# Performance work log

Measured on AMD Instinct MI355X. Metric: run time of the kernel, lower is better.

## Reference

```python
import jax, jax.numpy as jnp
import numpy as np

B, S, D, H = 2, 2048, 1024, 16
DK = D // H
NEG = -1e9


def setup_inputs() -> dict:
    key = jax.random.key(0)
    ks = jax.random.split(key, 12)
    inp = {
        "query": jax.random.normal(ks[0], (B, S, D), jnp.float32),
        "key": jax.random.normal(ks[1], (B, S, D), jnp.float32),
        "value": jax.random.normal(ks[2], (B, S, D), jnp.float32),
        "mask": jax.random.randint(ks[3], (B, S), 0, 2, jnp.int32),
    }
    # 4 linears (q, k, v, out), each d_model x d_model with bias.
    scale = 1.0 / np.sqrt(D)
    for i, name in enumerate(["wq", "wk", "wv", "wo"]):
        inp[name] = jax.random.uniform(ks[4 + i], (D, D), jnp.float32, -scale, scale)
        inp["b" + name[1]] = jax.random.uniform(ks[8 + i], (D,), jnp.float32, -scale, scale)
    return inp


def _split_heads(x):  # [B,S,D] -> [B,H,S,DK]
    return x.reshape(B, S, H, DK).transpose(0, 2, 1, 3)


def reference(query, key, value, mask, wq, bq, wk, bk, wv, bv, wo, bo):
    q = _split_heads(query @ wq.T + bq)
    k = _split_heads(key @ wk.T + bk)
    v = _split_heads(value @ wv.T + bv)
    scores = jnp.einsum("bhqd,bhkd->bhqk", q, k) / jnp.sqrt(jnp.float32(DK))
    # mask: [B,S] -> [B,1,1,S]; masked_fill where mask == 0
    m = mask[:, None, None, :]
    scores = jnp.where(m == 0, NEG, scores)
    attn = jax.nn.softmax(scores, axis=-1)  # dropout p=0 (eval) -> identity
    x = jnp.einsum("bhqk,bhkd->bhqd", attn, v)
    x = x.transpose(0, 2, 1, 3).reshape(B, S, D)
    return x @ wo.T + bo
```

## Files before the change

### kernel.cpp

```cpp
#include <hip/hip_runtime.h>


typedef _Float16 f16;
typedef _Float16 f16x8 __attribute__((ext_vector_type(8)));
typedef _Float16 f16x4 __attribute__((ext_vector_type(4)));
typedef float f32x4 __attribute__((ext_vector_type(4)));

#define MFMA_F16(a, b, c) __builtin_amdgcn_mfma_f32_16x16x32_f16((a), (b), (c), 0, 0, 0)
#define MFMA16(a, b, c) __builtin_amdgcn_mfma_f32_16x16x16f16((a), (b), (c), 0, 0, 0)
#define L2E 1.44269504088896340736f

__device__ __forceinline__ void gld16(const void* g, void* l) {
    __builtin_amdgcn_global_load_lds(
        (__attribute__((address_space(1))) void*)(g),
        (__attribute__((address_space(3))) void*)(l), 16, 0, 0);
}

__global__ __launch_bounds__(256) void cvt_kernel(
    const float* __restrict__ q, const float* __restrict__ k,
    const float* __restrict__ v,
    const float* __restrict__ wq, const float* __restrict__ wk,
    const float* __restrict__ wv, const float* __restrict__ wo,
    f16* __restrict__ oq, f16* __restrict__ ok, f16* __restrict__ ov,
    f16* __restrict__ owq, f16* __restrict__ owk, f16* __restrict__ owv,
    f16* __restrict__ owo)
{
    const int z = blockIdx.y;
    const float* src;
    f16* dst;
    int n;
    switch (z) {
        case 0: src = q;  dst = oq;  n = 4194304; break;
        case 1: src = k;  dst = ok;  n = 4194304; break;
        case 2: src = v;  dst = ov;  n = 4194304; break;
        case 3: src = wq; dst = owq; n = 1048576; break;
        case 4: src = wk; dst = owk; n = 1048576; break;
        case 5: src = wv; dst = owv; n = 1048576; break;
        default: src = wo; dst = owo; n = 1048576; break;
    }
    int idx = (blockIdx.x * 256 + threadIdx.x) * 8;
    if (idx >= n) return;
    float4 a = *(const float4*)(src + idx);
    float4 b = *(const float4*)(src + idx + 4);
    f16x8 h = { (f16)a.x, (f16)a.y, (f16)a.z, (f16)a.w,
                (f16)b.x, (f16)b.y, (f16)b.z, (f16)b.w };
    *(f16x8*)(dst + idx) = h;
}

__global__ __launch_bounds__(256) void proj_qkv_kernel(
    const f16* __restrict__ xq, const f16* __restrict__ xk,
    const f16* __restrict__ xv,
    const f16* __restrict__ wqh, const f16* __restrict__ wkh,
    const f16* __restrict__ wvh,
    const float* __restrict__ bq, const float* __restrict__ bk,
    const float* __restrict__ bv,
    f16* __restrict__ qh, f16* __restrict__ kh, f16* __restrict__ vt)
{
    const int z = blockIdx.z;
    const f16* X = (z == 0) ? xq : (z == 1) ? xk : xv;
    const f16* W = (z == 0) ? wqh : (z == 1) ? wkh : wvh;
    const float* bias = (z == 0) ? bq : (z == 1) ? bk : bv;
    const f16* P0 = (z < 2) ? W : X;
    const f16* P1 = (z < 2) ? X : W;

    __shared__ __align__(16) f16 As[128 * 64];
    __shared__ __align__(16) f16 Bs[128 * 64];

    const int t = threadIdx.x;
    const int wave = t >> 6, lane = t & 63, quad = lane >> 4, l15 = lane & 15;
    const int m_base = (wave >> 1) * 64, n_base = (wave & 1) * 64;
    const int blockM = (z < 2) ? blockIdx.x * 128 : blockIdx.y * 128;
    const int blockN = (z < 2) ? blockIdx.y * 128 : blockIdx.x * 128;

    const int srow = lane >> 3;
    const int sblk = (lane & 7) ^ srow;

    f32x4 acc[4][4];
#pragma unroll
    for (int mt = 0; mt < 4; mt++)
#pragma unroll
        for (int nt = 0; nt < 4; nt++)
            acc[mt][nt] = (f32x4){0.f, 0.f, 0.f, 0.f};

    for (int k0 = 0; k0 < 1024; k0 += 64) {
        __syncthreads();
#pragma unroll
        for (int j = 0; j < 4; j++) {
            int r0 = wave * 32 + j * 8;
            gld16(&P0[(size_t)(blockM + r0 + srow) * 1024 + k0 + sblk * 8],
                  &As[r0 * 64]);
            gld16(&P1[(size_t)(blockN + r0 + srow) * 1024 + k0 + sblk * 8],
                  &Bs[r0 * 64]);
        }
        __syncthreads();

#pragma unroll
        for (int c = 0; c < 2; c++) {
            f16x8 af[4], bf[4];
#pragma unroll
            for (int mt = 0; mt < 4; mt++)
                af[mt] = *(const f16x8*)(&As[(m_base + mt * 16 + l15) * 64 +
                                             (((c * 4 + quad) ^ (l15 & 7)) << 3)]);
#pragma unroll
            for (int nt = 0; nt < 4; nt++)
                bf[nt] = *(const f16x8*)(&Bs[(n_base + nt * 16 + l15) * 64 +
                                             (((c * 4 + quad) ^ (l15 & 7)) << 3)]);
#pragma unroll
            for (int mt = 0; mt < 4; mt++)
#pragma unroll
                for (int nt = 0; nt < 4; nt++)
                    acc[mt][nt] = MFMA_F16(af[mt], bf[nt], acc[mt][nt]);
        }
    }

    if (z < 2) {
        f16* o = (z == 0) ? qh : kh;
        const float scale = (z == 0) ? 0.125f * L2E : 1.0f;
#pragma unroll
        for (int mt = 0; mt < 4; mt++) {
            int j0 = blockM + m_base + mt * 16 + quad * 4;
            float4 b4 = *(const float4*)(&bias[j0]);
            int h = j0 >> 6, dk = j0 & 63;
#pragma unroll
            for (int nt = 0; nt < 4; nt++) {
                int s_g = blockN + n_base + nt * 16 + l15;
                int b = s_g >> 11, s = s_g & 2047;
                f16x4 pk = { (f16)((acc[mt][nt][0] + b4.x) * scale),
                             (f16)((acc[mt][nt][1] + b4.y) * scale),
                             (f16)((acc[mt][nt][2] + b4.z) * scale),
                             (f16)((acc[mt][nt][3] + b4.w) * scale) };
                *(f16x4*)(&o[(((size_t)(b * 16 + h) * 2048 + s) << 6) + dk]) = pk;
            }
        }
    } else {
        float bv_[4];
#pragma unroll
        for (int nt = 0; nt < 4; nt++)
            bv_[nt] = bias[blockN + n_base + nt * 16 + l15];
#pragma unroll
        for (int mt = 0; mt < 4; mt++) {
            int row0 = blockM + m_base + mt * 16 + quad * 4;
            int b = row0 >> 11, s0 = row0 & 2047;
#pragma unroll
            for (int nt = 0; nt < 4; nt++) {
                int col_g = blockN + n_base + nt * 16 + l15;
                int h = col_g >> 6, dk = col_g & 63;
                f16x4 pk = { (f16)(acc[mt][nt][0] + bv_[nt]),
                             (f16)(acc[mt][nt][1] + bv_[nt]),
                             (f16)(acc[mt][nt][2] + bv_[nt]),
                             (f16)(acc[mt][nt][3] + bv_[nt]) };
                *(f16x4*)(&vt[((size_t)((b * 16 + h) * 64 + dk) << 11) + s0]) = pk;
            }
        }
    }
}

__global__ __launch_bounds__(256) void flash_kernel(
    const f16* __restrict__ qh, const f16* __restrict__ kh,
    const f16* __restrict__ vt, const int* __restrict__ mask,
    f16* __restrict__ ctx)
{
    __shared__ __align__(16) f16 Ks[64 * 64];
    __shared__ __align__(16) f16 Vts[64 * 64];
    __shared__ float bias_s[64];

    const int t = threadIdx.x;
    const int wave = t >> 6, lane = t & 63, quad = lane >> 4, l15 = lane & 15;
    const int bh = blockIdx.y;
    const int b = bh >> 4, h = bh & 15;
    const int q0 = blockIdx.x * 128;

    const f16* qbase = qh + (size_t)bh * (2048 * 64);
    const f16* kbase = kh + (size_t)bh * (2048 * 64);
    const f16* vbase = vt + (size_t)bh * (64 * 2048);

    f16x8 qf[2][2];
#pragma unroll
    for (int cb = 0; cb < 2; cb++) {
        int qrow = q0 + wave * 32 + cb * 16 + l15;
        qf[cb][0] = *(const f16x8*)(&qbase[qrow * 64 + quad * 8]);
        qf[cb][1] = *(const f16x8*)(&qbase[qrow * 64 + 32 + quad * 8]);
    }

    f32x4 O[2][4];
#pragma unroll
    for (int cb = 0; cb < 2; cb++)
#pragma unroll
        for (int n = 0; n < 4; n++) O[cb][n] = (f32x4){0.f, 0.f, 0.f, 0.f};
    float l_part[2] = {0.f, 0.f};

    const int sr = t >> 3;
    const int sb = t & 7;

    for (int kt = 0; kt < 32; kt++) {
        __syncthreads();
        const int key0 = kt * 64;
#pragma unroll
        for (int p = 0; p < 2; p++) {
            int row = p * 32 + sr;
            int pb = (sb ^ (row & 7)) << 3;
            *(f16x8*)(&Ks[row * 64 + pb]) =
                *(const f16x8*)(&kbase[(key0 + row) * 64 + sb * 8]);
            *(f16x8*)(&Vts[row * 64 + pb]) =
                *(const f16x8*)(&vbase[row * 2048 + key0 + sb * 8]);
        }
        if (t < 64)
            bias_s[t] = (mask[b * 2048 + key0 + t] == 0) ? -1.0e9f : 0.0f;
        __syncthreads();

        f32x4 sc[2][4];
#pragma unroll
        for (int nt = 0; nt < 4; nt++) {
            const f16* krow = &Ks[(nt * 16 + l15) * 64];
            f16x8 kf0 = *(const f16x8*)(&krow[(quad ^ (l15 & 7)) << 3]);
            f16x8 kf1 = *(const f16x8*)(&krow[((quad + 4) ^ (l15 & 7)) << 3]);
            float4 b4 = *(const float4*)(&bias_s[nt * 16 + quad * 4]);
#pragma unroll
            for (int cb = 0; cb < 2; cb++) {
                f32x4 z4 = (f32x4){b4.x, b4.y, b4.z, b4.w};
                z4 = MFMA_F16(kf0, qf[cb][0], z4);
                sc[cb][nt] = MFMA_F16(kf1, qf[cb][1], z4);
            }
        }

        f16x4 pf[2][4];
#pragma unroll
        for (int cb = 0; cb < 2; cb++) {
            float rs = 0.f;
#pragma unroll
            for (int nt = 0; nt < 4; nt++)
#pragma unroll
                for (int i = 0; i < 4; i++) {
                    float p = exp2f(sc[cb][nt][i]);
                    rs += p;
                    pf[cb][nt][i] = (f16)p;
                }
            l_part[cb] += rs;
        }

#pragma unroll
        for (int nto = 0; nto < 4; nto++) {
            const f16* vrow = &Vts[(nto * 16 + l15) * 64];
#pragma unroll
            for (int nt = 0; nt < 4; nt++) {
                f16x4 vf = *(const f16x4*)(&vrow[
                    (((nt * 2 + (quad >> 1)) ^ (l15 & 7)) << 3) + (quad & 1) * 4]);
                O[0][nto] = MFMA16(vf, pf[0][nt], O[0][nto]);
                O[1][nto] = MFMA16(vf, pf[1][nt], O[1][nto]);
            }
        }
    }

#pragma unroll
    for (int cb = 0; cb < 2; cb++) {
        float l = l_part[cb];
        l += __shfl_xor(l, 16);
        l += __shfl_xor(l, 32);
        const float inv_l = 1.0f / l;
        int qrow = q0 + wave * 32 + cb * 16 + l15;
#pragma unroll
        for (int nto = 0; nto < 4; nto++) {
            f16x4 pk = { (f16)(O[cb][nto][0] * inv_l),
                         (f16)(O[cb][nto][1] * inv_l),
                         (f16)(O[cb][nto][2] * inv_l),
                         (f16)(O[cb][nto][3] * inv_l) };
            *(f16x4*)(&ctx[(size_t)(b * 2048 + qrow) * 1024 + h * 64 +
                           nto * 16 + quad * 4]) = pk;
        }
    }
}

__global__ __launch_bounds__(256) void proj_out_kernel(
    const f16* __restrict__ ctx, const f16* __restrict__ woh,
    const float* __restrict__ bo, float* __restrict__ out)
{
    __shared__ __align__(16) f16 As[128 * 64];
    __shared__ __align__(16) f16 Bs[128 * 64];

    const int t = threadIdx.x;
    const int wave = t >> 6, lane = t & 63, quad = lane >> 4, l15 = lane & 15;
    const int m_base = (wave >> 1) * 64, n_base = (wave & 1) * 64;
    const int blockM = blockIdx.y * 128, blockN = blockIdx.x * 128;

    const int srow = lane >> 3;
    const int sblk = (lane & 7) ^ srow;

    f32x4 acc[4][4];
#pragma unroll
    for (int mt = 0; mt < 4; mt++)
#pragma unroll
        for (int nt = 0; nt < 4; nt++)
            acc[mt][nt] = (f32x4){0.f, 0.f, 0.f, 0.f};

    for (int k0 = 0; k0 < 1024; k0 += 64) {
        __syncthreads();
#pragma unroll
        for (int j = 0; j < 4; j++) {
            int r0 = wave * 32 + j * 8;
            gld16(&ctx[(size_t)(blockM + r0 + srow) * 1024 + k0 + sblk * 8],
                  &As[r0 * 64]);
            gld16(&woh[(size_t)(blockN + r0 + srow) * 1024 + k0 + sblk * 8],
                  &Bs[r0 * 64]);
        }
        __syncthreads();

#pragma unroll
        for (int c = 0; c < 2; c++) {
            f16x8 af[4], bf[4];
#pragma unroll
            for (int mt = 0; mt < 4; mt++)
                af[mt] = *(const f16x8*)(&As[(m_base + mt * 16 + l15) * 64 +
                                             (((c * 4 + quad) ^ (l15 & 7)) << 3)]);
#pragma unroll
            for (int nt = 0; nt < 4; nt++)
                bf[nt] = *(const f16x8*)(&Bs[(n_base + nt * 16 + l15) * 64 +
                                             (((c * 4 + quad) ^ (l15 & 7)) << 3)]);
#pragma unroll
            for (int mt = 0; mt < 4; mt++)
#pragma unroll
                for (int nt = 0; nt < 4; nt++)
                    acc[mt][nt] = MFMA_F16(af[mt], bf[nt], acc[mt][nt]);
        }
    }

    float bo_[4];
#pragma unroll
    for (int nt = 0; nt < 4; nt++)
        bo_[nt] = bo[blockN + n_base + nt * 16 + l15];

#pragma unroll
    for (int mt = 0; mt < 4; mt++) {
        int row0 = blockM + m_base + mt * 16 + quad * 4;
#pragma unroll
        for (int nt = 0; nt < 4; nt++) {
            int col_g = blockN + n_base + nt * 16 + l15;
#pragma unroll
            for (int i = 0; i < 4; i++)
                out[(size_t)(row0 + i) * 1024 + col_g] = acc[mt][nt][i] + bo_[nt];
        }
    }
}

extern "C" void kernel_launch(void* const* d_in, const int* in_sizes, int n_in,
                              void* d_out, int out_size, void* d_ws, size_t ws_size,
                              hipStream_t stream) {
    const float* query = (const float*)d_in[0];
    const float* key_  = (const float*)d_in[1];
    const float* value = (const float*)d_in[2];
    const int*   mask  = (const int*)d_in[3];
    const float* wq = (const float*)d_in[4];
    const float* bq = (const float*)d_in[5];
    const float* wk = (const float*)d_in[6];
    const float* bk = (const float*)d_in[7];
    const float* wv = (const float*)d_in[8];
    const float* bv = (const float*)d_in[9];
    const float* wo = (const float*)d_in[10];
    const float* bo = (const float*)d_in[11];
    float* out = (float*)d_out;

    f16* xq  = (f16*)d_ws;
    f16* xk  = xq  + 4194304;
    f16* xv  = xk  + 4194304;
    f16* wqh = xv  + 4194304;
    f16* wkh = wqh + 1048576;
    f16* wvh = wkh + 1048576;
    f16* woh = wvh + 1048576;
    f16* qh  = woh + 1048576;
    f16* kh  = qh  + 4194304;
    f16* vt  = kh  + 4194304;
    f16* ctx = xq;

    cvt_kernel<<<dim3(2048, 7), 256, 0, stream>>>(
        query, key_, value, wq, wk, wv, wo, xq, xk, xv, wqh, wkh, wvh, woh);
    proj_qkv_kernel<<<dim3(8, 32, 3), 256, 0, stream>>>(
        xq, xk, xv, wqh, wkh, wvh, bq, bk, bv, qh, kh, vt);
    flash_kernel<<<dim3(16, 32), 256, 0, stream>>>(qh, kh, vt, mask, ctx);
    proj_out_kernel<<<dim3(8, 32), 256, 0, stream>>>(ctx, woh, bo, out);
}
```

Before: 260.0 us.

## Swap grid axes for L2 locality, use direct-to-LDS loads and precompute mask bias

Transposes the launch grids of the projection and attention kernels so consecutive blocks share the same weight or head data, which is meant to improve L2 reuse. The flash kernel now stages K and V tiles with global_load_lds instead of going through registers. It also builds the whole mask bias row (2048 floats) in LDS once per block rather than once per key tile. This costs extra LDS, which may reduce occupancy.

```diff
diff --git a/kernel.cpp b/kernel.cpp
--- a/kernel.cpp
+++ b/kernel.cpp
@@ -69,8 +69,8 @@
     const int t = threadIdx.x;
     const int wave = t >> 6, lane = t & 63, quad = lane >> 4, l15 = lane & 15;
     const int m_base = (wave >> 1) * 64, n_base = (wave & 1) * 64;
-    const int blockM = (z < 2) ? blockIdx.x * 128 : blockIdx.y * 128;
-    const int blockN = (z < 2) ? blockIdx.y * 128 : blockIdx.x * 128;
+    const int blockM = (z < 2) ? blockIdx.y * 128 : blockIdx.x * 128;
+    const int blockN = (z < 2) ? blockIdx.x * 128 : blockIdx.y * 128;
 
     const int srow = lane >> 3;
     const int sblk = (lane & 7) ^ srow;
@@ -162,17 +162,23 @@
 {
     __shared__ __align__(16) f16 Ks[64 * 64];
     __shared__ __align__(16) f16 Vts[64 * 64];
-    __shared__ float bias_s[64];
+    __shared__ float bias_all[2048];
 
     const int t = threadIdx.x;
     const int wave = t >> 6, lane = t & 63, quad = lane >> 4, l15 = lane & 15;
-    const int bh = blockIdx.y;
+    const int bh = blockIdx.x;
     const int b = bh >> 4, h = bh & 15;
-    const int q0 = blockIdx.x * 128;
+    const int q0 = blockIdx.y * 128;
 
     const f16* qbase = qh + (size_t)bh * (2048 * 64);
     const f16* kbase = kh + (size_t)bh * (2048 * 64);
     const f16* vbase = vt + (size_t)bh * (64 * 2048);
+
+#pragma unroll
+    for (int j = 0; j < 8; j++) {
+        int i = j * 256 + t;
+        bias_all[i] = (mask[b * 2048 + i] == 0) ? -1.0e9f : 0.0f;
+    }
 
     f16x8 qf[2][2];
 #pragma unroll
@@ -189,23 +195,19 @@
         for (int n = 0; n < 4; n++) O[cb][n] = (f32x4){0.f, 0.f, 0.f, 0.f};
     float l_part[2] = {0.f, 0.f};
 
-    const int sr = t >> 3;
-    const int sb = t & 7;
+    const int srow8 = lane >> 3;
+    const int sblk = (lane & 7) ^ srow8;
 
     for (int kt = 0; kt < 32; kt++) {
         __syncthreads();
         const int key0 = kt * 64;
 #pragma unroll
         for (int p = 0; p < 2; p++) {
-            int row = p * 32 + sr;
-            int pb = (sb ^ (row & 7)) << 3;
-            *(f16x8*)(&Ks[row * 64 + pb]) =
-                *(const f16x8*)(&kbase[(key0 + row) * 64 + sb * 8]);
-            *(f16x8*)(&Vts[row * 64 + pb]) =
-                *(const f16x8*)(&vbase[row * 2048 + key0 + sb * 8]);
-        }
-        if (t < 64)
-            bias_s[t] = (mask[b * 2048 + key0 + t] == 0) ? -1.0e9f : 0.0f;
+            int r0 = p * 32 + wave * 8;
+            int row = r0 + srow8;
+            gld16(&kbase[(size_t)(key0 + row) * 64 + sblk * 8], &Ks[r0 * 64]);
+            gld16(&vbase[(size_t)row * 2048 + key0 + sblk * 8], &Vts[r0 * 64]);
+        }
         __syncthreads();
 
         f32x4 sc[2][4];
@@ -214,7 +216,7 @@
             const f16* krow = &Ks[(nt * 16 + l15) * 64];
             f16x8 kf0 = *(const f16x8*)(&krow[(quad ^ (l15 & 7)) << 3]);
             f16x8 kf1 = *(const f16x8*)(&krow[((quad + 4) ^ (l15 & 7)) << 3]);
-            float4 b4 = *(const float4*)(&bias_s[nt * 16 + quad * 4]);
+            float4 b4 = *(const float4*)(&bias_all[key0 + nt * 16 + quad * 4]);
 #pragma unroll
             for (int cb = 0; cb < 2; cb++) {
                 f32x4 z4 = (f32x4){b4.x, b4.y, b4.z, b4.w};
@@ -280,7 +282,8 @@
     const int t = threadIdx.x;
     const int wave = t >> 6, lane = t & 63, quad = lane >> 4, l15 = lane & 15;
     const int m_base = (wave >> 1) * 64, n_base = (wave & 1) * 64;
-    const int blockM = blockIdx.y * 128, blockN = blockIdx.x * 128;
+    const int blockM = blockIdx.x * 128;
+    const int blockN = blockIdx.y * 128;
 
     const int srow = lane >> 3;
     const int sblk = (lane & 7) ^ srow;
@@ -372,8 +375,8 @@
 
     cvt_kernel<<<dim3(2048, 7), 256, 0, stream>>>(
         query, key_, value, wq, wk, wv, wo, xq, xk, xv, wqh, wkh, wvh, woh);
-    proj_qkv_kernel<<<dim3(8, 32, 3), 256, 0, stream>>>(
+    proj_qkv_kernel<<<dim3(32, 8, 3), 256, 0, stream>>>(
         xq, xk, xv, wqh, wkh, wvh, bq, bk, bv, qh, kh, vt);
-    flash_kernel<<<dim3(16, 32), 256, 0, stream>>>(qh, kh, vt, mask, ctx);
-    proj_out_kernel<<<dim3(8, 32), 256, 0, stream>>>(ctx, woh, bo, out);
-}
+    flash_kernel<<<dim3(32, 16), 256, 0, stream>>>(qh, kh, vt, mask, ctx);
+    proj_out_kernel<<<dim3(32, 8), 256, 0, stream>>>(ctx, woh, bo, out);
+}
```

Result: faster. 242.3 us (-6.8%).
